# Kernel optimization log

Measured on AMD Instinct MI355X. Metric: run time of the kernel, lower is better.

The kernel has to match this reference:

```python
import jax, jax.numpy as jnp
import numpy as np

DIM_Q = 256
DIM_K = 256
DIM_V = 256
NUM_HEADS = 4


def setup_inputs() -> dict:
    key = jax.random.key(0)
    ks = jax.random.split(key, 12)
    B, NQ, NK = 4, 2048, 2048
    s_in = 1.0 / np.sqrt(DIM_Q)
    s_v = 1.0 / np.sqrt(DIM_V)
    return {
        "Q": jax.random.normal(ks[0], (B, NQ, DIM_Q), jnp.float32),
        "K": jax.random.normal(ks[1], (B, NK, DIM_K), jnp.float32),
        "Wq": jax.random.normal(ks[2], (DIM_V, DIM_Q), jnp.float32) * s_in,
        "bq": jnp.zeros((DIM_V,), jnp.float32),
        "Wk": jax.random.normal(ks[3], (DIM_V, DIM_K), jnp.float32) * s_in,
        "bk": jnp.zeros((DIM_V,), jnp.float32),
        "Wv": jax.random.normal(ks[4], (DIM_V, DIM_K), jnp.float32) * s_in,
        "bv": jnp.zeros((DIM_V,), jnp.float32),
        "Wo": jax.random.normal(ks[5], (DIM_V, DIM_V), jnp.float32) * s_v,
        "bo": jnp.zeros((DIM_V,), jnp.float32),
        "g0": jnp.ones((DIM_V,), jnp.float32),
        "b0": jnp.zeros((DIM_V,), jnp.float32),
        "g1": jnp.ones((DIM_V,), jnp.float32),
        "b1": jnp.zeros((DIM_V,), jnp.float32),
    }


def _layernorm(x, g, b, eps=1e-5):
    mu = jnp.mean(x, axis=-1, keepdims=True)
    var = jnp.mean(jnp.square(x - mu), axis=-1, keepdims=True)
    return (x - mu) * jax.lax.rsqrt(var + eps) * g + b


def _mab(Q, K, Wq, bq, Wk, bk, Wv, bv, Wo, bo, g0, b0, g1, b1):
    B, NQ, _ = Q.shape
    H = NUM_HEADS
    Dh = DIM_V // H  # head dim
    q = jnp.einsum("bqd,ed->bqe", Q, Wq) + bq  # (B,NQ,DV)
    k = jnp.einsum("bkd,ed->bke", K, Wk) + bk
    v = jnp.einsum("bkd,ed->bke", K, Wv) + bv
    # split heads: (B,S,H,Dh) -> (B,H,S,Dh)
    qh = q.reshape(B, NQ, H, Dh).transpose(0, 2, 1, 3)
    kh = k.reshape(B, -1, H, Dh).transpose(0, 2, 1, 3)
    vh = v.reshape(B, -1, H, Dh).transpose(0, 2, 1, 3)
    # NOTE: original scales by sqrt(dim_V), not sqrt(head_dim)
    scores = jnp.einsum("bhqd,bhkd->bhqk", qh, kh) / np.sqrt(DIM_V)
    A = jax.nn.softmax(scores, axis=-1)
    oh = qh + jnp.einsum("bhqk,bhkd->bhqd", A, vh)  # residual with projected Q
    O = oh.transpose(0, 2, 1, 3).reshape(B, NQ, DIM_V)
    O = _layernorm(O, g0, b0)
    O = O + jax.nn.relu(jnp.einsum("bqd,ed->bqe", O, Wo) + bo)
    O = _layernorm(O, g1, b1)
    return O


def reference(Q, K, Wq, bq, Wk, bk, Wv, bv, Wo, bo, g0, b0, g1, b1):
    return _mab(Q, K, Wq, bq, Wk, bk, Wv, bv, Wo, bo, g0, b0, g1, b1)
```

## Files before the change

kernel.cpp:

```cpp
#include <hip/hip_runtime.h>
#include <hip/hip_bf16.h>
#include <math.h>


typedef __attribute__((ext_vector_type(8))) short bf16x8;
typedef __attribute__((ext_vector_type(4))) float f32x4;

static __device__ __forceinline__ unsigned short f2bf(float x) {
  return __bfloat16_as_ushort(__float2bfloat16(x));
}
static __device__ __forceinline__ int pk2(float lo, float hi) {
  return (int)((unsigned)f2bf(lo) | ((unsigned)f2bf(hi) << 16));
}
static __device__ __forceinline__ float exp2_fast(float x) {
  float r; asm("v_exp_f32 %0, %1" : "=v"(r) : "v"(x)); return r;
}

#define SWZ(row, col) ((col) ^ (((row) & 7) << 3))

typedef unsigned short tile64_t[64][64];

__global__ __launch_bounds__(256, 2) void proj2_kernel(
    const float* __restrict__ Q, const float* __restrict__ K,
    const float* __restrict__ Wq, const float* __restrict__ bq,
    const float* __restrict__ Wk, const float* __restrict__ bk,
    const float* __restrict__ Wv, const float* __restrict__ bv,
    float* __restrict__ qout, unsigned short* __restrict__ kbf,
    unsigned short* __restrict__ vtb)
{
  __shared__ __align__(16) unsigned short Ab[64][256];
  __shared__ __align__(16) unsigned short Wb[64][64];
  const int tid = threadIdx.x;
  const int z = blockIdx.z;
  const int bm = blockIdx.y;

  const float* A    = (z == 0) ? Q  : K;
  const float* W    = (z == 0) ? Wq : ((z == 1) ? Wk : Wv);
  const float* bias = (z == 0) ? bq : ((z == 1) ? bk : bv);

  const int wid = tid >> 6, lane = tid & 63;
  const int l15 = lane & 15, g = lane >> 4;
  const int wr = wid >> 1, wc = wid & 1;
  const float* Ablk = A + (size_t)bm * 64 * 256;

  const int sr = tid >> 2, sc = (tid & 3) * 16;
  const int c0 = SWZ(sr, sc), c1 = SWZ(sr, sc + 8);

  #pragma unroll
  for (int kb = 0; kb < 4; ++kb) {
    const float* ap = Ablk + (size_t)sr*256 + kb*64 + sc;
    float4 a0 = *(const float4*)ap,       a1 = *(const float4*)(ap + 4);
    float4 a2 = *(const float4*)(ap + 8), a3 = *(const float4*)(ap + 12);
    int4 p0 = { pk2(a0.x,a0.y), pk2(a0.z,a0.w), pk2(a1.x,a1.y), pk2(a1.z,a1.w) };
    int4 p1 = { pk2(a2.x,a2.y), pk2(a2.z,a2.w), pk2(a3.x,a3.y), pk2(a3.z,a3.w) };
    *(int4*)&Ab[sr][kb*64 + c0] = p0;
    *(int4*)&Ab[sr][kb*64 + c1] = p1;
  }

  for (int bi = 0; bi < 2; ++bi) {
    const int bn = blockIdx.x + bi*2;
    const float* Wblk = W + (size_t)bn * 64 * 256;

    f32x4 acc[2][2];
    #pragma unroll
    for (int i = 0; i < 2; ++i)
      #pragma unroll
      for (int j = 0; j < 2; ++j)
        #pragma unroll
        for (int r = 0; r < 4; ++r) acc[i][j][r] = 0.f;

    for (int k0 = 0; k0 < 256; k0 += 64) {
      if (bi | k0) __syncthreads();
      {
        const float* wp = Wblk + (size_t)sr*256 + k0 + sc;
        float4 w0 = *(const float4*)wp,       w1 = *(const float4*)(wp + 4);
        float4 w2 = *(const float4*)(wp + 8), w3 = *(const float4*)(wp + 12);
        int4 p0 = { pk2(w0.x,w0.y), pk2(w0.z,w0.w), pk2(w1.x,w1.y), pk2(w1.z,w1.w) };
        int4 p1 = { pk2(w2.x,w2.y), pk2(w2.z,w2.w), pk2(w3.x,w3.y), pk2(w3.z,w3.w) };
        *(int4*)&Wb[sr][c0] = p0;
        *(int4*)&Wb[sr][c1] = p1;
      }
      __syncthreads();

      __builtin_amdgcn_s_setprio(1);
      #pragma unroll
      for (int kc = 0; kc < 64; kc += 32) {
        bf16x8 af[2], bf_[2];
        #pragma unroll
        for (int i = 0; i < 2; ++i) {
          int ra = wr*32 + i*16 + l15;
          int rb = wc*32 + i*16 + l15;
          if (z == 2) {
            af[i]  = *(const bf16x8*)&Wb[ra][SWZ(ra, kc + g*8)];
            bf_[i] = *(const bf16x8*)&Ab[rb][k0 + SWZ(rb, kc + g*8)];
          } else {
            af[i]  = *(const bf16x8*)&Ab[ra][k0 + SWZ(ra, kc + g*8)];
            bf_[i] = *(const bf16x8*)&Wb[rb][SWZ(rb, kc + g*8)];
          }
        }
        #pragma unroll
        for (int i = 0; i < 2; ++i)
          #pragma unroll
          for (int j = 0; j < 2; ++j)
            acc[i][j] = __builtin_amdgcn_mfma_f32_16x16x32_bf16(af[i], bf_[j], acc[i][j], 0, 0, 0);
      }
      __builtin_amdgcn_s_setprio(0);
    }

    if (z == 2) {
      const int bvb = bm >> 5;
      const int n0 = (bm & 31) * 64 + wc*32;
      #pragma unroll
      for (int di = 0; di < 2; ++di)
        #pragma unroll
        for (int r = 0; r < 4; ++r) {
          int d = wr*32 + di*16 + g*4 + r;
          float bvs = bias[bn*64 + d];
          #pragma unroll
          for (int ni = 0; ni < 2; ++ni) {
            float c = acc[di][ni][r] + bvs;
            vtb[((size_t)(bvb*4 + bn)*64 + d)*2048 + n0 + ni*16 + l15] = f2bf(c);
          }
        }
    } else {
      const int gm = bm*64 + wr*32, ge = bn*64 + wc*32;
      float bv0 = bias[ge + l15], bv1 = bias[ge + 16 + l15];
      #pragma unroll
      for (int mi = 0; mi < 2; ++mi)
        #pragma unroll
        for (int r = 0; r < 4; ++r) {
          int row = gm + mi*16 + g*4 + r;
          #pragma unroll
          for (int ei = 0; ei < 2; ++ei) {
            float c = acc[mi][ei][r] + (ei ? bv1 : bv0);
            if (z == 0) qout[(size_t)row*256 + ge + ei*16 + l15] = c;
            else        kbf [(size_t)row*256 + ge + ei*16 + l15] = f2bf(c);
          }
        }
    }
  }
}

__global__ __launch_bounds__(512, 4) void attn_mfma6(
    const float* __restrict__ q,
    const unsigned short* __restrict__ kb,
    const unsigned short* __restrict__ vt,
    float* __restrict__ o)
{
  extern __shared__ __align__(16) char smem_dyn[];
  tile64_t* Ks = (tile64_t*)smem_dyn;
  tile64_t* Vt = (tile64_t*)(smem_dyn + 32768);

  const int tid = threadIdx.x;
  const int wid = tid >> 6;
  const int grp = wid >> 2;
  const int w4  = wid & 3;
  const int lane = tid & 63;
  const int l15 = lane & 15;
  const int g = lane >> 4;
  const int lin = blockIdx.x;
  const int xcd = lin & 7, idx = lin >> 3;
  const int bh = xcd * 2 + (idx >> 5);
  const int qb = idx & 31;
  const int b = bh >> 2, h = bh & 3;

  const float qscale = 0.0625f * 1.44269504089f;
  bf16x8 qf[2];
  {
    const float* qp = q + ((size_t)(b*2048 + qb*64 + w4*16 + l15))*256 + h*64;
    #pragma unroll
    for (int ds_ = 0; ds_ < 2; ++ds_) {
      union { bf16x8 v; unsigned short s[8]; } tmp;
      #pragma unroll
      for (int j = 0; j < 8; ++j) tmp.s[j] = f2bf(qp[ds_*32 + g*8 + j] * qscale);
      qf[ds_] = tmp.v;
    }
  }

  const int gt = tid & 255;
  const int sr = gt >> 2, sc = (gt & 3) * 16;
  const int c0 = SWZ(sr, sc), c1 = SWZ(sr, sc + 8);
  const unsigned short* kgp = kb + ((size_t)(b*2048 + grp*1024 + sr))*256 + h*64 + sc;
  const unsigned short* vgp = vt + ((size_t)bh*64 + sr)*2048 + grp*1024 + sc;

  f32x4 oa[4];
  #pragma unroll
  for (int mt = 0; mt < 4; ++mt)
    #pragma unroll
    for (int r = 0; r < 4; ++r) oa[mt][r] = 0.f;
  float l_ = 0.f;

  {
    int4 k0_ = *(const int4*)kgp, k1_ = *(const int4*)(kgp + 8);
    int4 v0_ = *(const int4*)vgp, v1_ = *(const int4*)(vgp + 8);
    *(int4*)&Ks[grp*2+0][sr][c0] = k0_;  *(int4*)&Ks[grp*2+0][sr][c1] = k1_;
    *(int4*)&Vt[grp*2+0][sr][c0] = v0_;  *(int4*)&Vt[grp*2+0][sr][c1] = v1_;
  }
  int4 kA0 = *(const int4*)(kgp + (size_t)64*256);
  int4 kA1 = *(const int4*)(kgp + (size_t)64*256 + 8);
  int4 vA0 = *(const int4*)(vgp + 64);
  int4 vA1 = *(const int4*)(vgp + 64 + 8);
  __syncthreads();

  for (int kt = 0; kt < 16; ++kt) {
    const int cur = kt & 1;
    const tile64_t& Kc = Ks[grp*2 + cur];
    const tile64_t& Vc = Vt[grp*2 + cur];

    f32x4 sa[4];
    #pragma unroll
    for (int mt = 0; mt < 4; ++mt)
      #pragma unroll
      for (int r = 0; r < 4; ++r) sa[mt][r] = 0.f;
    __builtin_amdgcn_s_setprio(1);
    #pragma unroll
    for (int ds_ = 0; ds_ < 2; ++ds_) {
      #pragma unroll
      for (int mt = 0; mt < 4; ++mt) {
        bf16x8 af = *(const bf16x8*)&Kc[mt*16 + l15][SWZ(l15, ds_*32 + g*8)];
        sa[mt] = __builtin_amdgcn_mfma_f32_16x16x32_bf16(af, qf[ds_], sa[mt], 0, 0, 0);
      }
    }
    __builtin_amdgcn_s_setprio(0);

    float ps = 0.f;
    unsigned pk01[4], pk23[4];
    #pragma unroll
    for (int mt = 0; mt < 4; ++mt) {
      float p0 = exp2_fast(sa[mt][0]);
      float p1 = exp2_fast(sa[mt][1]);
      float p2 = exp2_fast(sa[mt][2]);
      float p3 = exp2_fast(sa[mt][3]);
      ps += (p0 + p1) + (p2 + p3);
      pk01[mt] = (unsigned)pk2(p0, p1);
      pk23[mt] = (unsigned)pk2(p2, p3);
    }
    ps += __shfl_xor(ps, 16, 64);
    ps += __shfl_xor(ps, 32, 64);
    l_ += ps;

    __builtin_amdgcn_s_setprio(1);
    #pragma unroll
    for (int ks_ = 0; ks_ < 2; ++ks_) {
      unsigned a0 = pk01[2*ks_], b0 = pk01[2*ks_ + 1];
      unsigned a1 = pk23[2*ks_], b1 = pk23[2*ks_ + 1];
      asm volatile("v_permlane32_swap_b32 %0, %1" : "+v"(a0), "+v"(b0));
      asm volatile("v_permlane16_swap_b32 %0, %1" : "+v"(a0), "+v"(b0));
      asm volatile("v_permlane32_swap_b32 %0, %1" : "+v"(a1), "+v"(b1));
      asm volatile("v_permlane16_swap_b32 %0, %1" : "+v"(a1), "+v"(b1));
      int4 pw = { (int)a0, (int)a1, (int)b0, (int)b1 };
      bf16x8 pf = __builtin_bit_cast(bf16x8, pw);
      #pragma unroll
      for (int mt = 0; mt < 4; ++mt) {
        bf16x8 vf = *(const bf16x8*)&Vc[mt*16 + l15][SWZ(l15, ks_*32 + g*8)];
        oa[mt] = __builtin_amdgcn_mfma_f32_16x16x32_bf16(vf, pf, oa[mt], 0, 0, 0);
      }
    }
    __builtin_amdgcn_s_setprio(0);

    if (kt < 15) {
      *(int4*)&Ks[grp*2+(cur^1)][sr][c0] = kA0;
      *(int4*)&Ks[grp*2+(cur^1)][sr][c1] = kA1;
      *(int4*)&Vt[grp*2+(cur^1)][sr][c0] = vA0;
      *(int4*)&Vt[grp*2+(cur^1)][sr][c1] = vA1;
      if (kt < 14) {
        const unsigned short* kn = kgp + (size_t)(kt + 2) * 64 * 256;
        const unsigned short* vn = vgp + (kt + 2) * 64;
        kA0 = *(const int4*)kn;  kA1 = *(const int4*)(kn + 8);
        vA0 = *(const int4*)vn;  vA1 = *(const int4*)(vn + 8);
      }
    }
    __syncthreads();
  }

  float* cob = (float*)smem_dyn;
  float* cml = (float*)(smem_dyn + 32768);
  const int ci = w4*64 + lane;
  if (grp == 1) {
    #pragma unroll
    for (int mt = 0; mt < 4; ++mt)
      #pragma unroll
      for (int r = 0; r < 4; ++r) cob[(mt*4 + r)*256 + ci] = oa[mt][r];
    cml[ci] = l_;
  }
  __syncthreads();
  if (grp == 0) {
    float linv = 1.0f / (l_ + cml[ci]);
    float* op = o + ((size_t)(b*2048 + qb*64 + w4*16 + l15))*256 + h*64;
    #pragma unroll
    for (int mt = 0; mt < 4; ++mt) {
      int dbase = mt*16 + g*4;
      float4 qv = *(const float4*)(op + dbase);
      float4 st;
      st.x = qv.x + (oa[mt][0] + cob[(mt*4+0)*256 + ci]) * linv;
      st.y = qv.y + (oa[mt][1] + cob[(mt*4+1)*256 + ci]) * linv;
      st.z = qv.z + (oa[mt][2] + cob[(mt*4+2)*256 + ci]) * linv;
      st.w = qv.w + (oa[mt][3] + cob[(mt*4+3)*256 + ci]) * linv;
      *(float4*)(op + dbase) = st;
    }
  }
}

__global__ __launch_bounds__(512) void fused_out(
    const float* __restrict__ x, const float* __restrict__ Wo,
    const float* __restrict__ bo,
    const float* __restrict__ g0v, const float* __restrict__ b0v,
    const float* __restrict__ g1v, const float* __restrict__ b1v,
    float* __restrict__ y)
{
  __shared__ __align__(16) unsigned short As[32][256];
  __shared__ __align__(16) unsigned short Ws[256][64];
  __shared__ float mu_[32], rs_[32];
  float* P = (float*)&Ws[0][0];

  const int tid = threadIdx.x;
  const int w = tid >> 6, lane = tid & 63;
  const int l15 = lane & 15, g = lane >> 4;
  const int r0 = blockIdx.x * 32;

  {
    float4 g4 = *(const float4*)(g0v + lane*4);
    float4 b4 = *(const float4*)(b0v + lane*4);
    #pragma unroll
    for (int rr = 0; rr < 4; ++rr) {
      int m = w*4 + rr;
      const float* xr = x + (size_t)(r0 + m) * 256;
      float4 v = *(const float4*)(xr + lane*4);
      float s = v.x + v.y + v.z + v.w;
      #pragma unroll
      for (int mk = 1; mk <= 32; mk <<= 1) s += __shfl_xor(s, mk, 64);
      float mu = s * (1.0f/256.0f);
      float dx = v.x-mu, dy = v.y-mu, dz = v.z-mu, dw = v.w-mu;
      float qq = dx*dx + dy*dy + dz*dz + dw*dw;
      #pragma unroll
      for (int mk = 1; mk <= 32; mk <<= 1) qq += __shfl_xor(qq, mk, 64);
      float rstd = rsqrtf(qq * (1.0f/256.0f) + 1e-5f);
      if (lane == 0) { mu_[m] = mu; rs_[m] = rstd; }
      float nx = dx*rstd*g4.x + b4.x;
      float ny = dy*rstd*g4.y + b4.y;
      float nz = dz*rstd*g4.z + b4.z;
      float nw = dw*rstd*g4.w + b4.w;
      int2 pv = { pk2(nx, ny), pk2(nz, nw) };
      *(int2*)&As[m][SWZ(m, lane*4)] = pv;
    }
  }
  __syncthreads();

  const int m0 = (w >> 2) * 16;
  const int e0 = (w & 3) * 64;
  f32x4 acc4[4];
  #pragma unroll
  for (int j = 0; j < 4; ++j)
    #pragma unroll
    for (int r = 0; r < 4; ++r) acc4[j][r] = 0.f;

  for (int k0 = 0; k0 < 256; k0 += 64) {
    if (k0) __syncthreads();
    {
      const int ch = tid & 7;
      const int er = tid >> 3;
      #pragma unroll
      for (int p = 0; p < 4; ++p) {
        int e = p*64 + er;
        const float* wp = Wo + (size_t)e*256 + k0 + ch*8;
        float4 u0 = *(const float4*)wp;
        float4 u1 = *(const float4*)(wp + 4);
        int4 pk = { pk2(u0.x,u0.y), pk2(u0.z,u0.w), pk2(u1.x,u1.y), pk2(u1.z,u1.w) };
        *(int4*)&Ws[e][SWZ(e, ch*8)] = pk;
      }
    }
    __syncthreads();
    __builtin_amdgcn_s_setprio(1);
    #pragma unroll
    for (int ds_ = 0; ds_ < 2; ++ds_) {
      int ma = m0 + l15;
      bf16x8 af = *(const bf16x8*)&As[ma][SWZ(ma, k0 + ds_*32 + g*8)];
      #pragma unroll
      for (int j = 0; j < 4; ++j) {
        int er = e0 + j*16 + l15;
        bf16x8 bfv = *(const bf16x8*)&Ws[er][SWZ(er, ds_*32 + g*8)];
        acc4[j] = __builtin_amdgcn_mfma_f32_16x16x32_bf16(af, bfv, acc4[j], 0, 0, 0);
      }
    }
    __builtin_amdgcn_s_setprio(0);
  }
  __syncthreads();

  #pragma unroll
  for (int j = 0; j < 4; ++j) {
    int e = e0 + j*16 + l15;
    float bov = bo[e], g0e = g0v[e], b0e = b0v[e];
    #pragma unroll
    for (int r = 0; r < 4; ++r) {
      int m = m0 + g*4 + r;
      float xv = x[(size_t)(r0 + m)*256 + e];
      float resv = (xv - mu_[m]) * rs_[m] * g0e + b0e;
      float val = acc4[j][r] + bov;
      P[m*256 + e] = resv + fmaxf(val, 0.f);
    }
  }
  __syncthreads();

  {
    float4 g4 = *(const float4*)(g1v + lane*4);
    float4 b4 = *(const float4*)(b1v + lane*4);
    #pragma unroll
    for (int rr = 0; rr < 4; ++rr) {
      int m = w*4 + rr;
      float4 v = *(const float4*)&P[m*256 + lane*4];
      float s = v.x + v.y + v.z + v.w;
      #pragma unroll
      for (int mk = 1; mk <= 32; mk <<= 1) s += __shfl_xor(s, mk, 64);
      float mu = s * (1.0f/256.0f);
      float dx = v.x-mu, dy = v.y-mu, dz = v.z-mu, dw = v.w-mu;
      float qq = dx*dx + dy*dy + dz*dz + dw*dw;
      #pragma unroll
      for (int mk = 1; mk <= 32; mk <<= 1) qq += __shfl_xor(qq, mk, 64);
      float rstd = rsqrtf(qq * (1.0f/256.0f) + 1e-5f);
      float4 o;
      o.x = dx*rstd*g4.x + b4.x; o.y = dy*rstd*g4.y + b4.y;
      o.z = dz*rstd*g4.z + b4.z; o.w = dw*rstd*g4.w + b4.w;
      *(float4*)(y + (size_t)(r0 + m)*256 + lane*4) = o;
    }
  }
}

extern "C" void kernel_launch(void* const* d_in, const int* in_sizes, int n_in,
                              void* d_out, int out_size, void* d_ws, size_t ws_size,
                              hipStream_t stream) {
  const float* Q  = (const float*)d_in[0];
  const float* K  = (const float*)d_in[1];
  const float* Wq = (const float*)d_in[2];
  const float* bq = (const float*)d_in[3];
  const float* Wk = (const float*)d_in[4];
  const float* bk = (const float*)d_in[5];
  const float* Wv = (const float*)d_in[6];
  const float* bv = (const float*)d_in[7];
  const float* Wo = (const float*)d_in[8];
  const float* bo = (const float*)d_in[9];
  const float* g0 = (const float*)d_in[10];
  const float* b0 = (const float*)d_in[11];
  const float* g1 = (const float*)d_in[12];
  const float* b1 = (const float*)d_in[13];
  float* out = (float*)d_out;

  const size_t SZ = (size_t)4 * 2048 * 256;
  if (ws_size < 2 * SZ * sizeof(unsigned short)) return;

  unsigned short* kbf = (unsigned short*)d_ws;
  unsigned short* vtb = kbf + SZ;

  const int ATTN_LDS = 65536;
  hipFuncSetAttribute((const void*)attn_mfma6,
                      hipFuncAttributeMaxDynamicSharedMemorySize, ATTN_LDS);

  proj2_kernel<<<dim3(2, 128, 3), dim3(256), 0, stream>>>(
      Q, K, Wq, bq, Wk, bk, Wv, bv, out, kbf, vtb);
  attn_mfma6<<<dim3(512), dim3(512), ATTN_LDS, stream>>>(out, kbf, vtb, out);
  fused_out<<<dim3(256), dim3(512), 0, stream>>>(out, Wo, bo, g0, b0, g1, b1, out);
}
```

Before: 68.01 us.

## Software-pipeline attention loop so next tile's QK overlaps current PV

The attention main loop is unrolled by two with separate score and probability registers for alternating tiles. The QK^T MFMAs of the next K tile are issued before the PV MFMAs of the current tile, and the softmax exponentials are placed between the LDS staging writes. The aim is to give the scheduler independent MFMA and transcendental work to interleave within each wave, hiding exp and permlane latency behind matrix ops. In exchange it needs more registers for the double score buffers and twice as many barriers per tile pair.

```diff
diff --git a/kernel.cpp b/kernel.cpp
--- a/kernel.cpp
+++ b/kernel.cpp
@@ -141,7 +141,65 @@
   }
 }
 
-__global__ __launch_bounds__(512, 4) void attn_mfma6(
+#define ATT_SOFTMAX(SA, PK01, PK23, LACC)                                    \
+  do {                                                                       \
+    float ps_ = 0.f;                                                         \
+    _Pragma("unroll")                                                        \
+    for (int mt = 0; mt < 4; ++mt) {                                         \
+      float p0 = exp2_fast(SA[mt][0]);                                       \
+      float p1 = exp2_fast(SA[mt][1]);                                       \
+      float p2 = exp2_fast(SA[mt][2]);                                       \
+      float p3 = exp2_fast(SA[mt][3]);                                       \
+      ps_ += (p0 + p1) + (p2 + p3);                                          \
+      PK01[mt] = (unsigned)pk2(p0, p1);                                      \
+      PK23[mt] = (unsigned)pk2(p2, p3);                                      \
+    }                                                                        \
+    ps_ += __shfl_xor(ps_, 16, 64);                                          \
+    ps_ += __shfl_xor(ps_, 32, 64);                                          \
+    LACC += ps_;                                                             \
+  } while (0)
+
+#define ATT_QK(SA, KBUF)                                                     \
+  do {                                                                       \
+    _Pragma("unroll")                                                        \
+    for (int mt = 0; mt < 4; ++mt)                                           \
+      _Pragma("unroll")                                                      \
+      for (int r = 0; r < 4; ++r) SA[mt][r] = 0.f;                           \
+    __builtin_amdgcn_s_setprio(1);                                           \
+    _Pragma("unroll")                                                        \
+    for (int ds_ = 0; ds_ < 2; ++ds_) {                                      \
+      _Pragma("unroll")                                                      \
+      for (int mt = 0; mt < 4; ++mt) {                                       \
+        bf16x8 af = *(const bf16x8*)&KBUF[mt*16 + l15][SWZ(l15, ds_*32 + g*8)]; \
+        SA[mt] = __builtin_amdgcn_mfma_f32_16x16x32_bf16(af, qf[ds_], SA[mt], 0, 0, 0); \
+      }                                                                      \
+    }                                                                        \
+    __builtin_amdgcn_s_setprio(0);                                           \
+  } while (0)
+
+#define ATT_PV(PK01, PK23, VBUF)                                             \
+  do {                                                                       \
+    __builtin_amdgcn_s_setprio(1);                                           \
+    _Pragma("unroll")                                                        \
+    for (int ks_ = 0; ks_ < 2; ++ks_) {                                      \
+      unsigned a0 = PK01[2*ks_], b0 = PK01[2*ks_ + 1];                       \
+      unsigned a1 = PK23[2*ks_], b1 = PK23[2*ks_ + 1];                       \
+      asm volatile("v_permlane32_swap_b32 %0, %1" : "+v"(a0), "+v"(b0));     \
+      asm volatile("v_permlane16_swap_b32 %0, %1" : "+v"(a0), "+v"(b0));     \
+      asm volatile("v_permlane32_swap_b32 %0, %1" : "+v"(a1), "+v"(b1));     \
+      asm volatile("v_permlane16_swap_b32 %0, %1" : "+v"(a1), "+v"(b1));     \
+      int4 pw = { (int)a0, (int)a1, (int)b0, (int)b1 };                      \
+      bf16x8 pf = __builtin_bit_cast(bf16x8, pw);                            \
+      _Pragma("unroll")                                                      \
+      for (int mt = 0; mt < 4; ++mt) {                                       \
+        bf16x8 vf = *(const bf16x8*)&VBUF[mt*16 + l15][SWZ(l15, ks_*32 + g*8)]; \
+        oa[mt] = __builtin_amdgcn_mfma_f32_16x16x32_bf16(vf, pf, oa[mt], 0, 0, 0); \
+      }                                                                      \
+    }                                                                        \
+    __builtin_amdgcn_s_setprio(0);                                           \
+  } while (0)
+
+__global__ __launch_bounds__(512, 4) void attn_mfma10(
     const float* __restrict__ q,
     const unsigned short* __restrict__ kb,
     const unsigned short* __restrict__ vt,
@@ -183,6 +241,11 @@
   const unsigned short* kgp = kb + ((size_t)(b*2048 + grp*1024 + sr))*256 + h*64 + sc;
   const unsigned short* vgp = vt + ((size_t)bh*64 + sr)*2048 + grp*1024 + sc;
 
+  const tile64_t& K0 = Ks[grp*2 + 0];
+  const tile64_t& K1 = Ks[grp*2 + 1];
+  const tile64_t& V0 = Vt[grp*2 + 0];
+  const tile64_t& V1 = Vt[grp*2 + 1];
+
   f32x4 oa[4];
   #pragma unroll
   for (int mt = 0; mt < 4; ++mt)
@@ -202,77 +265,46 @@
   int4 vA1 = *(const int4*)(vgp + 64 + 8);
   __syncthreads();
 
-  for (int kt = 0; kt < 16; ++kt) {
-    const int cur = kt & 1;
-    const tile64_t& Kc = Ks[grp*2 + cur];
-    const tile64_t& Vc = Vt[grp*2 + cur];
-
-    f32x4 sa[4];
-    #pragma unroll
-    for (int mt = 0; mt < 4; ++mt)
-      #pragma unroll
-      for (int r = 0; r < 4; ++r) sa[mt][r] = 0.f;
-    __builtin_amdgcn_s_setprio(1);
-    #pragma unroll
-    for (int ds_ = 0; ds_ < 2; ++ds_) {
-      #pragma unroll
-      for (int mt = 0; mt < 4; ++mt) {
-        bf16x8 af = *(const bf16x8*)&Kc[mt*16 + l15][SWZ(l15, ds_*32 + g*8)];
-        sa[mt] = __builtin_amdgcn_mfma_f32_16x16x32_bf16(af, qf[ds_], sa[mt], 0, 0, 0);
-      }
-    }
-    __builtin_amdgcn_s_setprio(0);
-
-    float ps = 0.f;
-    unsigned pk01[4], pk23[4];
-    #pragma unroll
-    for (int mt = 0; mt < 4; ++mt) {
-      float p0 = exp2_fast(sa[mt][0]);
-      float p1 = exp2_fast(sa[mt][1]);
-      float p2 = exp2_fast(sa[mt][2]);
-      float p3 = exp2_fast(sa[mt][3]);
-      ps += (p0 + p1) + (p2 + p3);
-      pk01[mt] = (unsigned)pk2(p0, p1);
-      pk23[mt] = (unsigned)pk2(p2, p3);
-    }
-    ps += __shfl_xor(ps, 16, 64);
-    ps += __shfl_xor(ps, 32, 64);
-    l_ += ps;
-
-    __builtin_amdgcn_s_setprio(1);
-    #pragma unroll
-    for (int ks_ = 0; ks_ < 2; ++ks_) {
-      unsigned a0 = pk01[2*ks_], b0 = pk01[2*ks_ + 1];
-      unsigned a1 = pk23[2*ks_], b1 = pk23[2*ks_ + 1];
-      asm volatile("v_permlane32_swap_b32 %0, %1" : "+v"(a0), "+v"(b0));
-      asm volatile("v_permlane16_swap_b32 %0, %1" : "+v"(a0), "+v"(b0));
-      asm volatile("v_permlane32_swap_b32 %0, %1" : "+v"(a1), "+v"(b1));
-      asm volatile("v_permlane16_swap_b32 %0, %1" : "+v"(a1), "+v"(b1));
-      int4 pw = { (int)a0, (int)a1, (int)b0, (int)b1 };
-      bf16x8 pf = __builtin_bit_cast(bf16x8, pw);
-      #pragma unroll
-      for (int mt = 0; mt < 4; ++mt) {
-        bf16x8 vf = *(const bf16x8*)&Vc[mt*16 + l15][SWZ(l15, ks_*32 + g*8)];
-        oa[mt] = __builtin_amdgcn_mfma_f32_16x16x32_bf16(vf, pf, oa[mt], 0, 0, 0);
-      }
-    }
-    __builtin_amdgcn_s_setprio(0);
-
-    if (kt < 15) {
-      *(int4*)&Ks[grp*2+(cur^1)][sr][c0] = kA0;
-      *(int4*)&Ks[grp*2+(cur^1)][sr][c1] = kA1;
-      *(int4*)&Vt[grp*2+(cur^1)][sr][c0] = vA0;
-      *(int4*)&Vt[grp*2+(cur^1)][sr][c1] = vA1;
-      if (kt < 14) {
-        const unsigned short* kn = kgp + (size_t)(kt + 2) * 64 * 256;
-        const unsigned short* vn = vgp + (kt + 2) * 64;
+  f32x4 saA[4], saB[4];
+  unsigned pkA01[4], pkA23[4], pkB01[4], pkB23[4];
+  ATT_QK(saA, K0);
+
+  for (int tt = 0; tt < 8; ++tt) {
+    const int tA = 2*tt;
+    __syncthreads();
+    {
+      *(int4*)&Ks[grp*2+1][sr][c0] = kA0;  *(int4*)&Ks[grp*2+1][sr][c1] = kA1;
+      *(int4*)&Vt[grp*2+1][sr][c0] = vA0;  *(int4*)&Vt[grp*2+1][sr][c1] = vA1;
+    }
+    if (tt < 7) {
+      const unsigned short* kn = kgp + (size_t)(tA + 2) * 64 * 256;
+      const unsigned short* vn = vgp + (tA + 2) * 64;
+      kA0 = *(const int4*)kn;  kA1 = *(const int4*)(kn + 8);
+      vA0 = *(const int4*)vn;  vA1 = *(const int4*)(vn + 8);
+    }
+    ATT_SOFTMAX(saA, pkA01, pkA23, l_);
+    __syncthreads();
+    ATT_QK(saB, K1);
+    ATT_PV(pkA01, pkA23, V0);
+
+    __syncthreads();
+    if (tt < 7) {
+      *(int4*)&Ks[grp*2+0][sr][c0] = kA0;  *(int4*)&Ks[grp*2+0][sr][c1] = kA1;
+      *(int4*)&Vt[grp*2+0][sr][c0] = vA0;  *(int4*)&Vt[grp*2+0][sr][c1] = vA1;
+      if (tt < 7) {
+        const unsigned short* kn = kgp + (size_t)(tA + 3) * 64 * 256;
+        const unsigned short* vn = vgp + (tA + 3) * 64;
         kA0 = *(const int4*)kn;  kA1 = *(const int4*)(kn + 8);
         vA0 = *(const int4*)vn;  vA1 = *(const int4*)(vn + 8);
       }
     }
+    ATT_SOFTMAX(saB, pkB01, pkB23, l_);
     __syncthreads();
-  }
-
+    if (tt < 7) ATT_QK(saA, K0);
+    ATT_PV(pkB01, pkB23, V1);
+  }
+
+  __syncthreads();
   float* cob = (float*)smem_dyn;
   float* cml = (float*)(smem_dyn + 32768);
   const int ci = w4*64 + lane;
@@ -451,11 +483,11 @@
   unsigned short* vtb = kbf + SZ;
 
   const int ATTN_LDS = 65536;
-  hipFuncSetAttribute((const void*)attn_mfma6,
+  hipFuncSetAttribute((const void*)attn_mfma10,
                       hipFuncAttributeMaxDynamicSharedMemorySize, ATTN_LDS);
 
   proj2_kernel<<<dim3(2, 128, 3), dim3(256), 0, stream>>>(
       Q, K, Wq, bq, Wk, bk, Wv, bv, out, kbf, vtb);
-  attn_mfma6<<<dim3(512), dim3(512), ATTN_LDS, stream>>>(out, kbf, vtb, out);
+  attn_mfma10<<<dim3(512), dim3(512), ATTN_LDS, stream>>>(out, kbf, vtb, out);
   fused_out<<<dim3(256), dim3(512), 0, stream>>>(out, Wo, bo, g0, b0, g1, b1, out);
 }
```

After: 67.02 us. No clear change (-1.5%).

## Switch attention kernel to 32x32x16 MFMA tiles with 256-thread blocks

Applied to the files above, without the earlier changes.

Rewrites the attention inner loops to use 32x32x16 bf16 MFMA instructions, so each wave owns 32 queries and the full 64-key tile, instead of 16x16x32 MFMAs over 16 queries. Block size is halved to 256 threads (4 waves, two key-split groups of two query-waves). Each thread now stages 4 vectors per tile instead of 2, and the cross-group reduction layout is redone for the new accumulator mapping. The larger MFMA shape cuts LDS fragment reads per FLOP and shuffle work, at the cost of more registers per wave and fewer waves per block to hide latency.

```diff
diff --git a/kernel.cpp b/kernel.cpp
--- a/kernel.cpp
+++ b/kernel.cpp
@@ -5,6 +5,7 @@
 
 typedef __attribute__((ext_vector_type(8))) short bf16x8;
 typedef __attribute__((ext_vector_type(4))) float f32x4;
+typedef __attribute__((ext_vector_type(16))) float f32x16;
 
 static __device__ __forceinline__ unsigned short f2bf(float x) {
   return __bfloat16_as_ushort(__float2bfloat16(x));
@@ -141,7 +142,7 @@
   }
 }
 
-__global__ __launch_bounds__(512, 4) void attn_mfma6(
+__global__ __launch_bounds__(256, 2) void attn_mfma11(
     const float* __restrict__ q,
     const unsigned short* __restrict__ kb,
     const unsigned short* __restrict__ vt,
@@ -153,11 +154,11 @@
 
   const int tid = threadIdx.x;
   const int wid = tid >> 6;
-  const int grp = wid >> 2;
-  const int w4  = wid & 3;
+  const int grp = wid >> 1;
+  const int qw  = wid & 1;
   const int lane = tid & 63;
-  const int l15 = lane & 15;
-  const int g = lane >> 4;
+  const int l31 = lane & 31;
+  const int hi  = lane >> 5;
   const int lin = blockIdx.x;
   const int xcd = lin & 7, idx = lin >> 3;
   const int bh = xcd * 2 + (idx >> 5);
@@ -165,41 +166,44 @@
   const int b = bh >> 2, h = bh & 3;
 
   const float qscale = 0.0625f * 1.44269504089f;
-  bf16x8 qf[2];
+  bf16x8 qf[4];
   {
-    const float* qp = q + ((size_t)(b*2048 + qb*64 + w4*16 + l15))*256 + h*64;
-    #pragma unroll
-    for (int ds_ = 0; ds_ < 2; ++ds_) {
+    const float* qp = q + ((size_t)(b*2048 + qb*64 + qw*32 + l31))*256 + h*64;
+    #pragma unroll
+    for (int step = 0; step < 4; ++step) {
       union { bf16x8 v; unsigned short s[8]; } tmp;
       #pragma unroll
-      for (int j = 0; j < 8; ++j) tmp.s[j] = f2bf(qp[ds_*32 + g*8 + j] * qscale);
-      qf[ds_] = tmp.v;
-    }
-  }
-
-  const int gt = tid & 255;
-  const int sr = gt >> 2, sc = (gt & 3) * 16;
-  const int c0 = SWZ(sr, sc), c1 = SWZ(sr, sc + 8);
-  const unsigned short* kgp = kb + ((size_t)(b*2048 + grp*1024 + sr))*256 + h*64 + sc;
-  const unsigned short* vgp = vt + ((size_t)bh*64 + sr)*2048 + grp*1024 + sc;
-
-  f32x4 oa[4];
-  #pragma unroll
-  for (int mt = 0; mt < 4; ++mt)
-    #pragma unroll
-    for (int r = 0; r < 4; ++r) oa[mt][r] = 0.f;
+      for (int j = 0; j < 8; ++j)
+        tmp.s[j] = f2bf(qp[step*16 + hi*8 + j] * qscale);
+      qf[step] = tmp.v;
+    }
+  }
+
+  const int gt = tid & 127;
+  const int sr = gt >> 1;
+  const int scb = (gt & 1) * 32;
+  int cols[4];
+  #pragma unroll
+  for (int i = 0; i < 4; ++i) cols[i] = SWZ(sr, scb + 8*i);
+  const unsigned short* kgp = kb + ((size_t)(b*2048 + grp*1024 + sr))*256 + h*64 + scb;
+  const unsigned short* vgp = vt + ((size_t)(bh*64 + sr))*2048 + grp*1024 + scb;
+
+  f32x16 sa0, sa1, oa0, oa1;
+  #pragma unroll
+  for (int r = 0; r < 16; ++r) { oa0[r] = 0.f; oa1[r] = 0.f; }
   float l_ = 0.f;
 
-  {
-    int4 k0_ = *(const int4*)kgp, k1_ = *(const int4*)(kgp + 8);
-    int4 v0_ = *(const int4*)vgp, v1_ = *(const int4*)(vgp + 8);
-    *(int4*)&Ks[grp*2+0][sr][c0] = k0_;  *(int4*)&Ks[grp*2+0][sr][c1] = k1_;
-    *(int4*)&Vt[grp*2+0][sr][c0] = v0_;  *(int4*)&Vt[grp*2+0][sr][c1] = v1_;
-  }
-  int4 kA0 = *(const int4*)(kgp + (size_t)64*256);
-  int4 kA1 = *(const int4*)(kgp + (size_t)64*256 + 8);
-  int4 vA0 = *(const int4*)(vgp + 64);
-  int4 vA1 = *(const int4*)(vgp + 64 + 8);
+  #pragma unroll
+  for (int i = 0; i < 4; ++i) {
+    *(int4*)&Ks[grp*2+0][sr][cols[i]] = *(const int4*)(kgp + 8*i);
+    *(int4*)&Vt[grp*2+0][sr][cols[i]] = *(const int4*)(vgp + 8*i);
+  }
+  int4 kR[4], vR[4];
+  #pragma unroll
+  for (int i = 0; i < 4; ++i) {
+    kR[i] = *(const int4*)(kgp + (size_t)64*256 + 8*i);
+    vR[i] = *(const int4*)(vgp + 64 + 8*i);
+  }
   __syncthreads();
 
   for (int kt = 0; kt < 16; ++kt) {
@@ -207,96 +211,105 @@
     const tile64_t& Kc = Ks[grp*2 + cur];
     const tile64_t& Vc = Vt[grp*2 + cur];
 
-    f32x4 sa[4];
-    #pragma unroll
-    for (int mt = 0; mt < 4; ++mt)
-      #pragma unroll
-      for (int r = 0; r < 4; ++r) sa[mt][r] = 0.f;
+    #pragma unroll
+    for (int r = 0; r < 16; ++r) { sa0[r] = 0.f; sa1[r] = 0.f; }
     __builtin_amdgcn_s_setprio(1);
     #pragma unroll
-    for (int ds_ = 0; ds_ < 2; ++ds_) {
-      #pragma unroll
-      for (int mt = 0; mt < 4; ++mt) {
-        bf16x8 af = *(const bf16x8*)&Kc[mt*16 + l15][SWZ(l15, ds_*32 + g*8)];
-        sa[mt] = __builtin_amdgcn_mfma_f32_16x16x32_bf16(af, qf[ds_], sa[mt], 0, 0, 0);
-      }
+    for (int step = 0; step < 4; ++step) {
+      bf16x8 af0 = *(const bf16x8*)&Kc[l31     ][SWZ(l31, step*16 + hi*8)];
+      bf16x8 af1 = *(const bf16x8*)&Kc[32 + l31][SWZ(l31, step*16 + hi*8)];
+      sa0 = __builtin_amdgcn_mfma_f32_32x32x16_bf16(af0, qf[step], sa0, 0, 0, 0);
+      sa1 = __builtin_amdgcn_mfma_f32_32x32x16_bf16(af1, qf[step], sa1, 0, 0, 0);
     }
     __builtin_amdgcn_s_setprio(0);
 
     float ps = 0.f;
-    unsigned pk01[4], pk23[4];
-    #pragma unroll
-    for (int mt = 0; mt < 4; ++mt) {
-      float p0 = exp2_fast(sa[mt][0]);
-      float p1 = exp2_fast(sa[mt][1]);
-      float p2 = exp2_fast(sa[mt][2]);
-      float p3 = exp2_fast(sa[mt][3]);
-      ps += (p0 + p1) + (p2 + p3);
-      pk01[mt] = (unsigned)pk2(p0, p1);
-      pk23[mt] = (unsigned)pk2(p2, p3);
-    }
-    ps += __shfl_xor(ps, 16, 64);
+    unsigned pk0[8], pk1[8];
+    #pragma unroll
+    for (int r2 = 0; r2 < 8; ++r2) {
+      float p0 = exp2_fast(sa0[2*r2]);
+      float p1 = exp2_fast(sa0[2*r2 + 1]);
+      ps += p0 + p1;
+      pk0[r2] = (unsigned)pk2(p0, p1);
+    }
+    #pragma unroll
+    for (int r2 = 0; r2 < 8; ++r2) {
+      float p0 = exp2_fast(sa1[2*r2]);
+      float p1 = exp2_fast(sa1[2*r2 + 1]);
+      ps += p0 + p1;
+      pk1[r2] = (unsigned)pk2(p0, p1);
+    }
     ps += __shfl_xor(ps, 32, 64);
     l_ += ps;
 
     __builtin_amdgcn_s_setprio(1);
     #pragma unroll
-    for (int ks_ = 0; ks_ < 2; ++ks_) {
-      unsigned a0 = pk01[2*ks_], b0 = pk01[2*ks_ + 1];
-      unsigned a1 = pk23[2*ks_], b1 = pk23[2*ks_ + 1];
-      asm volatile("v_permlane32_swap_b32 %0, %1" : "+v"(a0), "+v"(b0));
-      asm volatile("v_permlane16_swap_b32 %0, %1" : "+v"(a0), "+v"(b0));
-      asm volatile("v_permlane32_swap_b32 %0, %1" : "+v"(a1), "+v"(b1));
-      asm volatile("v_permlane16_swap_b32 %0, %1" : "+v"(a1), "+v"(b1));
-      int4 pw = { (int)a0, (int)a1, (int)b0, (int)b1 };
+    for (int c = 0; c < 4; ++c) {
+      const int c1 = c & 1;
+      unsigned X, Z, Y, W;
+      if (c < 2) { X = pk0[4*c1+0]; Z = pk0[4*c1+1]; Y = pk0[4*c1+2]; W = pk0[4*c1+3]; }
+      else       { X = pk1[4*c1+0]; Z = pk1[4*c1+1]; Y = pk1[4*c1+2]; W = pk1[4*c1+3]; }
+      asm volatile("v_permlane32_swap_b32 %0, %1" : "+v"(X), "+v"(Y));
+      asm volatile("v_permlane32_swap_b32 %0, %1" : "+v"(Z), "+v"(W));
+      int4 pw = { (int)X, (int)Z, (int)Y, (int)W };
       bf16x8 pf = __builtin_bit_cast(bf16x8, pw);
-      #pragma unroll
-      for (int mt = 0; mt < 4; ++mt) {
-        bf16x8 vf = *(const bf16x8*)&Vc[mt*16 + l15][SWZ(l15, ks_*32 + g*8)];
-        oa[mt] = __builtin_amdgcn_mfma_f32_16x16x32_bf16(vf, pf, oa[mt], 0, 0, 0);
-      }
+      bf16x8 vf0 = *(const bf16x8*)&Vc[l31     ][SWZ(l31, c*16 + hi*8)];
+      bf16x8 vf1 = *(const bf16x8*)&Vc[32 + l31][SWZ(l31, c*16 + hi*8)];
+      oa0 = __builtin_amdgcn_mfma_f32_32x32x16_bf16(vf0, pf, oa0, 0, 0, 0);
+      oa1 = __builtin_amdgcn_mfma_f32_32x32x16_bf16(vf1, pf, oa1, 0, 0, 0);
     }
     __builtin_amdgcn_s_setprio(0);
 
     if (kt < 15) {
-      *(int4*)&Ks[grp*2+(cur^1)][sr][c0] = kA0;
-      *(int4*)&Ks[grp*2+(cur^1)][sr][c1] = kA1;
-      *(int4*)&Vt[grp*2+(cur^1)][sr][c0] = vA0;
-      *(int4*)&Vt[grp*2+(cur^1)][sr][c1] = vA1;
+      #pragma unroll
+      for (int i = 0; i < 4; ++i) {
+        *(int4*)&Ks[grp*2+(cur^1)][sr][cols[i]] = kR[i];
+        *(int4*)&Vt[grp*2+(cur^1)][sr][cols[i]] = vR[i];
+      }
       if (kt < 14) {
         const unsigned short* kn = kgp + (size_t)(kt + 2) * 64 * 256;
         const unsigned short* vn = vgp + (kt + 2) * 64;
-        kA0 = *(const int4*)kn;  kA1 = *(const int4*)(kn + 8);
-        vA0 = *(const int4*)vn;  vA1 = *(const int4*)(vn + 8);
+        #pragma unroll
+        for (int i = 0; i < 4; ++i) {
+          kR[i] = *(const int4*)(kn + 8*i);
+          vR[i] = *(const int4*)(vn + 8*i);
+        }
       }
     }
     __syncthreads();
   }
 
   float* cob = (float*)smem_dyn;
-  float* cml = (float*)(smem_dyn + 32768);
-  const int ci = w4*64 + lane;
+  float* cml = (float*)(smem_dyn + 16384);
+  const int qloc = qw*32 + l31;
   if (grp == 1) {
     #pragma unroll
-    for (int mt = 0; mt < 4; ++mt)
-      #pragma unroll
-      for (int r = 0; r < 4; ++r) cob[(mt*4 + r)*256 + ci] = oa[mt][r];
-    cml[ci] = l_;
+    for (int reg = 0; reg < 16; ++reg) {
+      int dr = (reg & 3) + 8*(reg >> 2) + 4*hi;
+      cob[(dr     )*64 + qloc] = oa0[reg];
+      cob[(dr + 32)*64 + qloc] = oa1[reg];
+    }
+    cml[qloc] = l_;
   }
   __syncthreads();
   if (grp == 0) {
-    float linv = 1.0f / (l_ + cml[ci]);
-    float* op = o + ((size_t)(b*2048 + qb*64 + w4*16 + l15))*256 + h*64;
-    #pragma unroll
-    for (int mt = 0; mt < 4; ++mt) {
-      int dbase = mt*16 + g*4;
-      float4 qv = *(const float4*)(op + dbase);
-      float4 st;
-      st.x = qv.x + (oa[mt][0] + cob[(mt*4+0)*256 + ci]) * linv;
-      st.y = qv.y + (oa[mt][1] + cob[(mt*4+1)*256 + ci]) * linv;
-      st.z = qv.z + (oa[mt][2] + cob[(mt*4+2)*256 + ci]) * linv;
-      st.w = qv.w + (oa[mt][3] + cob[(mt*4+3)*256 + ci]) * linv;
-      *(float4*)(op + dbase) = st;
+    float linv = 1.0f / (l_ + cml[qloc]);
+    float* op = o + ((size_t)(b*2048 + qb*64 + qloc))*256 + h*64;
+    #pragma unroll
+    for (int dt = 0; dt < 2; ++dt) {
+      #pragma unroll
+      for (int rr = 0; rr < 4; ++rr) {
+        const int dbase = dt*32 + 8*rr + 4*hi;
+        float4 qv = *(const float4*)(op + dbase);
+        float4 st;
+        #pragma unroll
+        for (int j = 0; j < 4; ++j) {
+          float own = dt ? oa1[4*rr + j] : oa0[4*rr + j];
+          float oth = cob[(dbase + j)*64 + qloc];
+          ((float*)&st)[j] = ((const float*)&qv)[j] + (own + oth) * linv;
+        }
+        *(float4*)(op + dbase) = st;
+      }
     }
   }
 }
@@ -451,11 +464,11 @@
   unsigned short* vtb = kbf + SZ;
 
   const int ATTN_LDS = 65536;
-  hipFuncSetAttribute((const void*)attn_mfma6,
+  hipFuncSetAttribute((const void*)attn_mfma11,
                       hipFuncAttributeMaxDynamicSharedMemorySize, ATTN_LDS);
 
   proj2_kernel<<<dim3(2, 128, 3), dim3(256), 0, stream>>>(
       Q, K, Wq, bq, Wk, bk, Wv, bv, out, kbf, vtb);
-  attn_mfma6<<<dim3(512), dim3(512), ATTN_LDS, stream>>>(out, kbf, vtb, out);
+  attn_mfma11<<<dim3(512), dim3(256), ATTN_LDS, stream>>>(out, kbf, vtb, out);
   fused_out<<<dim3(256), dim3(512), 0, stream>>>(out, Wo, bo, g0, b0, g1, b1, out);
 }
```

After: 123.7 us. 1.82x slower.
